# Kernel tuning notes

Hardware: AMD Instinct MI355X
Metric: run time of the kernel (lower is better)

## Reference

```python
import jax, jax.numpy as jnp
import numpy as np


def _gru(x, h, Wih, Whh, bih, bhh):
    # torch.nn.GRUCell math. x:(1,in), h:(1,H), Wih:(3H,in), Whh:(3H,H)
    gi = x @ Wih.T + bih
    gh = h @ Whh.T + bhh
    i_r, i_z, i_n = jnp.split(gi, 3, axis=-1)
    h_r, h_z, h_n = jnp.split(gh, 3, axis=-1)
    r = jax.nn.sigmoid(i_r + h_r)
    z = jax.nn.sigmoid(i_z + h_z)
    n = jnp.tanh(i_n + r * h_n)
    return (1.0 - z) * n + z * h


def _combine(S, Wa, ba, va):
    # SelfAttention.combine: additive attention over the stack axis.
    # S:(k,1,H), Wa:(H,A), ba:(A,), va:(A,)
    e = jnp.tanh(S @ Wa + ba) @ va          # (k,1) energies
    w = jax.nn.softmax(e, axis=0)            # softmax over stacked hidden states
    return jnp.sum(w[..., None] * S, axis=0)  # (1,H)


def setup_inputs() -> dict:
    key = jax.random.key(0)
    ks = jax.random.split(key, 20)
    T, F, H, A, L = 16384, 2048, 16, 64, 6
    G = 3 * H
    s = 0.1  # weight scale for numerical sanity
    return {
        "batch": jax.random.normal(ks[0], (T, 1, F), jnp.float32),
        "h0": jax.random.normal(ks[1], (L, 1, H), jnp.float32),
        "W_ih0": jax.random.normal(ks[2], (G, F), jnp.float32) * s,
        "W_hh0": jax.random.normal(ks[3], (G, H), jnp.float32) * s,
        "b_ih0": jax.random.normal(ks[4], (G,), jnp.float32) * s,
        "b_hh0": jax.random.normal(ks[5], (G,), jnp.float32) * s,
        "W_ih": jax.random.normal(ks[6], (L - 1, G, H), jnp.float32) * s,
        "W_hh": jax.random.normal(ks[7], (L - 1, G, H), jnp.float32) * s,
        "b_ih": jax.random.normal(ks[8], (L - 1, G), jnp.float32) * s,
        "b_hh": jax.random.normal(ks[9], (L - 1, G), jnp.float32) * s,
        "Wa": jax.random.normal(ks[10], (L, H, A), jnp.float32) * s,
        "ba": jax.random.normal(ks[11], (L, A), jnp.float32) * s,
        "va": jax.random.normal(ks[12], (L, A), jnp.float32) * s,
        "fc1_w": jax.random.normal(ks[13], (32, H), jnp.float32) * s,
        "fc1_b": jax.random.normal(ks[14], (32,), jnp.float32) * s,
        "fc2_w": jax.random.normal(ks[15], (1, 32), jnp.float32) * s,
        "fc2_b": jax.random.normal(ks[16], (1,), jnp.float32) * s,
    }


def reference(batch, h0, W_ih0, W_hh0, b_ih0, b_hh0, W_ih, W_hh, b_ih, b_hh,
              Wa, ba, va, fc1_w, fc1_b, fc2_w, fc2_b):
    L = Wa.shape[0]

    def step(h_s, x):
        # h_s: (L,1,H) carried hidden states, x: (1,F) current token
        inp = x.reshape(1, -1)
        new = []
        for l in range(L):
            if l == 0:
                inp = _gru(inp, h_s[0], W_ih0, W_hh0, b_ih0, b_hh0)
            else:
                inp = _gru(inp, h_s[l], W_ih[l - 1], W_hh[l - 1], b_ih[l - 1], b_hh[l - 1])
            new.append(inp)
        newS = jnp.stack(new)  # (L,1,H)
        # layer i attends over hidden states of layers i..L-1 (feedback combine)
        h_next = jnp.stack([_combine(newS[i:], Wa[i], ba[i], va[i]) for i in range(L)])
        top = h_next[-1].reshape(-1)  # (H,); dropout is identity in eval mode
        out = (top @ fc1_w.T + fc1_b) @ fc2_w.T + fc2_b  # (1,)
        return h_next, out

    _, outs = jax.lax.scan(step, h0, batch)
    return outs  # (T,1)
```

## Files before the change

kernel.cpp:

```cpp
#include <hip/hip_runtime.h>
#include <cstdint>
#include <cstddef>


#define TT 16384
#define FF 2048
#define HH 16
#define LL 6
#define GG 48
#define CHUNK 64
#define LOG2E 1.44269504088896340736f

__device__ float g_gi0p[(TT + CHUNK) * 64];

__device__ __forceinline__ float exp2_(float x) { return __builtin_amdgcn_exp2f(x); }
__device__ __forceinline__ float rcp_(float x) { return __builtin_amdgcn_rcpf(x); }
__device__ __forceinline__ float sig_n(float s) { return rcp_(1.f + exp2_(s)); }
__device__ __forceinline__ float tanh_p(float s) { return fmaf(-2.f, rcp_(exp2_(s) + 1.f), 1.f); }

#define MEMBAR() __asm__ __volatile__("" ::: "memory")

__device__ __forceinline__ float rdlane(float v, int l) {
  union { float f; int i; } a, b;
  a.f = v; b.i = __builtin_amdgcn_readlane(a.i, l); return b.f;
}
template <int CTRL>
__device__ __forceinline__ float dppf(float v) {
  union { float f; int i; } a, b;
  a.f = v; b.i = __builtin_amdgcn_mov_dpp(a.i, CTRL, 0xF, 0xF, true); return b.f;
}
template <int Q>
__device__ __forceinline__ float qbcast(float v) { return dppf<Q | (Q << 2) | (Q << 4) | (Q << 6)>(v); }

__device__ __forceinline__ float rowsum16(float v) {
  v += dppf<0xB1>(v);
  v += dppf<0x4E>(v);
  v += dppf<0x141>(v);
  v += dppf<0x140>(v);
  return v;
}
__device__ __forceinline__ float dot16r(const float (&w)[16], const float (&h)[16]) {
  float s0 = w[0] * h[0], s1 = w[1] * h[1], s2 = w[2] * h[2], s3 = w[3] * h[3];
#pragma unroll
  for (int k = 4; k < 16; k += 4) {
    s0 = fmaf(w[k], h[k], s0);       s1 = fmaf(w[k + 1], h[k + 1], s1);
    s2 = fmaf(w[k + 2], h[k + 2], s2); s3 = fmaf(w[k + 3], h[k + 3], s3);
  }
  return (s0 + s1) + (s2 + s3);
}
__device__ __forceinline__ float dot16i(const float (&w)[16], const float (&h)[16], float init) {
  float s0 = fmaf(w[0], h[0], init), s1 = w[1] * h[1], s2 = w[2] * h[2], s3 = w[3] * h[3];
#pragma unroll
  for (int k = 4; k < 16; k += 4) {
    s0 = fmaf(w[k], h[k], s0);       s1 = fmaf(w[k + 1], h[k + 1], s1);
    s2 = fmaf(w[k + 2], h[k + 2], s2); s3 = fmaf(w[k + 3], h[k + 3], s3);
  }
  return (s0 + s1) + (s2 + s3);
}

__device__ __forceinline__ void pollGE(int* f, int target) {
  while (__hip_atomic_load(f, __ATOMIC_ACQUIRE, __HIP_MEMORY_SCOPE_WORKGROUP) < target) {}
}
__device__ __forceinline__ void sigRel(int* f, int v) {
  __hip_atomic_store(f, v, __ATOMIC_RELAXED, __HIP_MEMORY_SCOPE_WORKGROUP);
}

__global__ __launch_bounds__(256) void gi0_gemm(const float* __restrict__ X,
                                                const float* __restrict__ W,
                                                const float* __restrict__ bias) {
  __shared__ float xs[64][132];
  __shared__ float ws[48][132];
  const int tid = threadIdx.x;
  const int t0 = blockIdx.x * 64;
  const int tg = tid & 15;
  const int tt = tid >> 4;
  float acc[4][3];
#pragma unroll
  for (int u = 0; u < 4; ++u)
#pragma unroll
    for (int v = 0; v < 3; ++v) acc[u][v] = 0.f;

  for (int k0 = 0; k0 < FF; k0 += 128) {
#pragma unroll
    for (int i = 0; i < 32; ++i) {
      int e = tid + 256 * i; int r = e >> 7, c = e & 127;
      xs[r][c] = X[(size_t)(t0 + r) * FF + k0 + c];
    }
#pragma unroll
    for (int i = 0; i < 24; ++i) {
      int e = tid + 256 * i; int r = e >> 7, c = e & 127;
      ws[r][c] = W[(size_t)r * FF + k0 + c];
    }
    __syncthreads();
#pragma unroll 8
    for (int c = 0; c < 128; ++c) {
      float x0 = xs[tt][c], x1 = xs[tt + 16][c], x2 = xs[tt + 32][c], x3 = xs[tt + 48][c];
      float w0 = ws[tg][c], w1 = ws[tg + 16][c], w2 = ws[tg + 32][c];
      acc[0][0] += x0 * w0; acc[0][1] += x0 * w1; acc[0][2] += x0 * w2;
      acc[1][0] += x1 * w0; acc[1][1] += x1 * w1; acc[1][2] += x1 * w2;
      acc[2][0] += x2 * w0; acc[2][1] += x2 * w1; acc[2][2] += x2 * w2;
      acc[3][0] += x3 * w0; acc[3][1] += x3 * w1; acc[3][2] += x3 * w2;
    }
    __syncthreads();
  }
  const float gsc3[3] = {-LOG2E, -LOG2E, 2.f * LOG2E};
#pragma unroll
  for (int u = 0; u < 4; ++u)
#pragma unroll
    for (int v = 0; v < 3; ++v)
      g_gi0p[(size_t)(t0 + tt + 16 * u) * 64 + tg * 4 + v] =
          (acc[u][v] + bias[tg + 16 * v]) * gsc3[v];
}

__global__ __launch_bounds__(512, 1) void fbrnn_scan(
    const float* __restrict__ h0,
    const float* __restrict__ Whh0, const float* __restrict__ bhh0,
    const float* __restrict__ Wih, const float* __restrict__ Whh,
    const float* __restrict__ bih, const float* __restrict__ bhh,
    const float* __restrict__ Wa, const float* __restrict__ ba,
    const float* __restrict__ va,
    const float* __restrict__ fc1w, const float* __restrict__ fc1b,
    const float* __restrict__ fc2w, const float* __restrict__ fc2b,
    float* __restrict__ out) {
  __shared__ __align__(16) float nsS[2][LL * HH];
  __shared__ __align__(16) float hS[2][5 * HH];
  __shared__ __align__(16) float ghS[2][5 * 64];
  __shared__ __align__(16) float nsOut[256 * HH];
  __shared__ __align__(16) float chunkS[2][CHUNK * 64];
  __shared__ int flagNs;
  __shared__ int cntC;
  __shared__ int flagChunk;
  __shared__ int flagOut;

  const int tid = threadIdx.x;
  const int wv = tid >> 6;
  const int lane = tid & 63;
  const int qg = lane & 3;
  const int kk = lane >> 2;
  const int k16 = lane & 15;
  const int gate = (qg < 3 ? qg : 2);
  const int G = gate * 16 + kk;
  const float gsc = (gate == 2) ? 2.f * LOG2E : -LOG2E;

  const bool isChain = (wv == 0);
  const bool isStream = (wv == 4);
  const bool isFc = (wv == 6);
  const bool isComb = !isChain && !isStream && !isFc;
  const int iw = (wv == 1) ? 0 : (wv == 2) ? 1 : (wv == 3) ? 2 : (wv == 7) ? 3 : 4;

  float WBih[5][16], bihR[5];
  float WB5[16];  float bhh5R = 0.f;
  float WaR[16], WhR[16];
  float baR = 0.f, vaR = 0.f, bhhR = 0.f;
  float fc1R[16];
  float fb1 = 0.f, fw2 = 0.f, fb2 = 0.f;

  if (isChain) {
#pragma unroll
    for (int l = 0; l < 5; ++l) {
#pragma unroll
      for (int k = 0; k < 16; ++k) WBih[l][k] = Wih[((l * GG) + G) * 16 + k] * gsc;
      bihR[l] = bih[l * GG + G] * gsc;
    }
#pragma unroll
    for (int k = 0; k < 16; ++k) WB5[k] = Whh[(4 * GG + G) * 16 + k] * gsc;
    bhh5R = bhh[4 * GG + G] * gsc;
  } else if (isComb) {
#pragma unroll
    for (int k = 0; k < 16; ++k) WaR[k] = Wa[(iw * 16 + k) * 64 + lane] * (2.f * LOG2E);
    baR = ba[iw * 64 + lane] * (2.f * LOG2E);
    vaR = va[iw * 64 + lane] * LOG2E;
    const float* wsrc = (iw == 0) ? (Whh0 + G * 16) : (Whh + ((iw - 1) * GG + G) * 16);
#pragma unroll
    for (int k = 0; k < 16; ++k) WhR[k] = wsrc[k] * gsc;
    bhhR = ((iw == 0) ? bhh0[G] : bhh[(iw - 1) * GG + G]) * gsc;
  } else if (isFc) {
    const int m = lane & 31;
#pragma unroll
    for (int k = 0; k < 16; ++k) fc1R[k] = fc1w[m * 16 + k];
    fb1 = fc1b[m]; fw2 = fc2w[m]; fb2 = fc2b[0];
  }

  if (tid == 0) { flagNs = 0; cntC = 0; flagChunk = 1; flagOut = 0; }

  float hv5 = 0.f, gh5reg = 0.f;
  if (isChain) {
    hv5 = h0[5 * 16 + kk];
    float hr[16];
#pragma unroll
    for (int k = 0; k < 16; ++k) hr[k] = h0[5 * 16 + k];
    gh5reg = dot16i(WB5, hr, bhh5R);
  } else if (isComb) {
    if (lane < 16) hS[1][iw * 16 + k16] = h0[iw * 16 + k16];
    float hr[16];
#pragma unroll
    for (int k = 0; k < 16; ++k) hr[k] = h0[iw * 16 + k];
    ghS[1][iw * 64 + lane] = dot16i(WhR, hr, bhhR);
  } else if (isStream) {
    const float4* src = (const float4*)g_gi0p;
    float4* dst = (float4*)(&chunkS[0][0]);
#pragma unroll
    for (int q = 0; q < 16; ++q) dst[q * 64 + lane] = src[q * 64 + lane];
  }
  __syncthreads();

  if (isStream) {
#pragma unroll 1
    for (int c = 1; c < 256; ++c) {
      if (c >= 2) pollGE(&flagNs, ((c - 1) * 64 - 1) * 8 + 1);
      const float4* src = (const float4*)(g_gi0p + ((size_t)c << 12));
      float4* dst = (float4*)(&chunkS[c & 1][0]);
#pragma unroll
      for (int q = 0; q < 16; ++q) dst[q * 64 + lane] = src[q * 64 + lane];
      MEMBAR();
      sigRel(&flagChunk, c + 1);
    }
    return;
  }

  if (isFc) {
    int fcc = 0;
#pragma unroll 1
    for (int t = 0; t < TT; ++t) {
      const int need = t * 8 + 6;
      if (fcc < need) {
        do {
          fcc = __hip_atomic_load(&flagNs, __ATOMIC_ACQUIRE, __HIP_MEMORY_SCOPE_WORKGROUP);
        } while (fcc < need);
      }
      const float4* np = (const float4*)(nsOut + (t & 255) * 16);
      float4 a0 = np[0], a1 = np[1], a2 = np[2], a3 = np[3];
      float nr[16] = {a0.x, a0.y, a0.z, a0.w, a1.x, a1.y, a1.z, a1.w,
                      a2.x, a2.y, a2.z, a2.w, a3.x, a3.y, a3.z, a3.w};
      float y = dot16i(fc1R, nr, fb1);
      float p = rowsum16(y * fw2);
      float o = rdlane(p, 0) + rdlane(p, 16) + fb2;
      if (lane == 0) out[t] = o;
      MEMBAR();
      sigRel(&flagOut, t + 1);
    }
    return;
  }

  if (isComb) {
    int fcache = 0;
#pragma unroll 1
    for (int t = 0; t < TT; ++t) {
      const int nb = t & 1;
      float S = 0.f, ha = 0.f, Pa = 0.f;
#pragma unroll
      for (int j = 0; j < 6; ++j) {
        if (j >= iw) {
          const int need = t * 8 + j + 1;
          if (fcache < need) {
            do {
              fcache = __hip_atomic_load(&flagNs, __ATOMIC_ACQUIRE, __HIP_MEMORY_SCOPE_WORKGROUP);
            } while (fcache < need);
          }
          const float4* np = (const float4*)(&nsS[nb][j * 16]);
          float4 a0 = np[0], a1 = np[1], a2 = np[2], a3 = np[3];
          float nr[16] = {a0.x, a0.y, a0.z, a0.w, a1.x, a1.y, a1.z, a1.w,
                          a2.x, a2.y, a2.z, a2.w, a3.x, a3.y, a3.z, a3.w};
          const float nsv = nsS[nb][j * 16 + k16];
          float u = dot16i(WaR, nr, baR);
          float pe = vaR * tanh_p(u);
          float P = dot16r(WhR, nr);
          float r = rowsum16(pe);
          float e = (rdlane(r, 0) + rdlane(r, 16)) + (rdlane(r, 32) + rdlane(r, 48));
          float w = exp2_(e);
          S += w; ha = fmaf(w, nsv, ha); Pa = fmaf(w, P, Pa);
        }
      }
      const float inv = rcp_(S);
      if (lane < 16) hS[nb][iw * 16 + k16] = ha * inv;
      ghS[nb][iw * 64 + lane] = fmaf(Pa, inv, bhhR);
      MEMBAR();
      if (lane == 0)
        __hip_atomic_fetch_add(&cntC, 1, __ATOMIC_RELAXED, __HIP_MEMORY_SCOPE_WORKGROUP);
    }
    return;
  }

  float gnext = chunkS[0][lane];
  float ns_sg[16];
  int ccache = 0;
#pragma unroll 1
  for (int t = 0; t < TT; ++t) {
    const int rb = (t + 1) & 1;
    const int wb = t & 1;

    const int cneed = 5 * t;
    if (ccache < cneed) {
      do {
        ccache = __hip_atomic_load(&cntC, __ATOMIC_ACQUIRE, __HIP_MEMORY_SCOPE_WORKGROUP);
      } while (ccache < cneed);
    }
    float ghv[6], hv[6];
#pragma unroll
    for (int l = 0; l < 5; ++l) { ghv[l] = ghS[rb][l * 64 + lane]; hv[l] = hS[rb][l * 16 + kk]; }
    ghv[5] = gh5reg; hv[5] = hv5;

    if ((t & 63) == 63) {
      const int cn = (t + 1) >> 6;
      if (cn < 256) pollGE(&flagChunk, cn + 1);
    }
    if ((t & 63) == 32) pollGE(&flagOut, t - 64);
    const float gpre = chunkS[((t + 1) >> 6) & 1][((t + 1) & 63) * 64 + lane];

    float ghb[6];
#pragma unroll
    for (int l = 1; l < 6; ++l) ghb[l] = ghv[l] + bihR[l - 1];

    float gi0v = gnext;
    float ns = 0.f;
#pragma unroll
    for (int l = 0; l < 6; ++l) {
      const float gh_g = ghv[l];
      const float s = (l == 0) ? (gi0v + gh_g) : dot16i(WBih[l - 1], ns_sg, ghb[l]);
      const float sg = sig_n(s);
      const float smg = s - gh_g;
      const float sr = qbcast<0>(sg);
      const float sz = qbcast<1>(sg);
      const float a = sz * hv[l];
      const float b = 1.f - sz;
      const float tq = tanh_p(fmaf(sr, gh_g, smg));
      ns = fmaf(tq, b, a);
      if (qg == 2) {
        nsS[wb][l * 16 + kk] = ns;
        if (l == 5) nsOut[(t & 255) * 16 + kk] = ns;
      }
      MEMBAR();
      if (l == 5 && lane == 0) sigRel(&flagNs, t * 8 + 6);
#pragma unroll
      for (int k = 0; k < 16; ++k) ns_sg[k] = rdlane(ns, 4 * k + 2);
      if (l < 5 && lane == 0) sigRel(&flagNs, t * 8 + l + 1);
    }
    hv5 = qbcast<2>(ns);
    gh5reg = dot16i(WB5, ns_sg, bhh5R);
    gnext = gpre;
  }
}

extern "C" void kernel_launch(void* const* d_in, const int* in_sizes, int n_in,
                              void* d_out, int out_size, void* d_ws, size_t ws_size,
                              hipStream_t stream) {
  const float* batch = (const float*)d_in[0];
  const float* h0    = (const float*)d_in[1];
  const float* Wih0  = (const float*)d_in[2];
  const float* Whh0  = (const float*)d_in[3];
  const float* bih0  = (const float*)d_in[4];
  const float* bhh0  = (const float*)d_in[5];
  const float* Wih   = (const float*)d_in[6];
  const float* Whh   = (const float*)d_in[7];
  const float* bih   = (const float*)d_in[8];
  const float* bhh   = (const float*)d_in[9];
  const float* Wa    = (const float*)d_in[10];
  const float* ba    = (const float*)d_in[11];
  const float* va    = (const float*)d_in[12];
  const float* fc1w  = (const float*)d_in[13];
  const float* fc1b  = (const float*)d_in[14];
  const float* fc2w  = (const float*)d_in[15];
  const float* fc2b  = (const float*)d_in[16];
  float* out = (float*)d_out;
  (void)in_sizes; (void)n_in; (void)out_size; (void)d_ws; (void)ws_size;

  gi0_gemm<<<TT / 64, 256, 0, stream>>>(batch, Wih0, bih0);
  fbrnn_scan<<<1, 512, 0, stream>>>(h0, Whh0, bhh0, Wih, Whh, bih, bhh,
                                    Wa, ba, va, fc1w, fc1b, fc2w, fc2b, out);
}
```

Baseline: 25.21 ms.

## Rebalance combine work across waves and replace counter sync with seqlock records

Combine waves for the lower layers now receive partial attention sums (over layers 0-2) that the fc and other waves compute early. The goal is to shorten the critical path after the last layer's state is produced. The shared counter plus separate hS/ghS buffers are replaced by float4 records with embedded generation tags, which the chain wave polls directly. A per-buffer gen5 flag signals the top-layer state. This removes the atomic fetch-add and the double-buffered read, but adds seqlock-style retry loops and more register pressure on the combine waves.

```diff
diff --git a/kernel.cpp b/kernel.cpp
--- a/kernel.cpp
+++ b/kernel.cpp
@@ -58,11 +58,33 @@
   return (s0 + s1) + (s2 + s3);
 }
 
+__device__ __forceinline__ int ldAcq(int* f) {
+  return __hip_atomic_load(f, __ATOMIC_ACQUIRE, __HIP_MEMORY_SCOPE_WORKGROUP);
+}
 __device__ __forceinline__ void pollGE(int* f, int target) {
-  while (__hip_atomic_load(f, __ATOMIC_ACQUIRE, __HIP_MEMORY_SCOPE_WORKGROUP) < target) {}
+  while (ldAcq(f) < target) {}
+}
+__device__ __forceinline__ void waitFlag(int* f, int& cache, int need) {
+  if (cache < need) { do { cache = ldAcq(f); } while (cache < need); }
 }
 __device__ __forceinline__ void sigRel(int* f, int v) {
   __hip_atomic_store(f, v, __ATOMIC_RELAXED, __HIP_MEMORY_SCOPE_WORKGROUP);
+}
+
+__device__ __forceinline__ void combBlock(const float4 A0, const float4 A1, const float4 A2,
+                                          const float4 A3, float nsv,
+                                          const float (&Wa)[16], float ba, float va,
+                                          const float (&Wh)[16],
+                                          float& S, float& ha, float& Pa) {
+  float nr[16] = {A0.x, A0.y, A0.z, A0.w, A1.x, A1.y, A1.z, A1.w,
+                  A2.x, A2.y, A2.z, A2.w, A3.x, A3.y, A3.z, A3.w};
+  float u = dot16i(Wa, nr, ba);
+  float P = dot16r(Wh, nr);
+  float pe = va * tanh_p(u);
+  float r = rowsum16(pe);
+  float e = (rdlane(r, 0) + rdlane(r, 16)) + (rdlane(r, 32) + rdlane(r, 48));
+  float w = exp2_(e);
+  S += w; ha = fmaf(w, nsv, ha); Pa = fmaf(w, P, Pa);
 }
 
 __global__ __launch_bounds__(256) void gi0_gemm(const float* __restrict__ X,
@@ -123,21 +145,20 @@
     const float* __restrict__ fc2w, const float* __restrict__ fc2b,
     float* __restrict__ out) {
   __shared__ __align__(16) float nsS[2][LL * HH];
-  __shared__ __align__(16) float hS[2][5 * HH];
-  __shared__ __align__(16) float ghS[2][5 * 64];
+  __shared__ __align__(16) float4 recS[5 * 64];
+  __shared__ __align__(16) float4 partS[3 * 64];
   __shared__ __align__(16) float nsOut[256 * HH];
   __shared__ __align__(16) float chunkS[2][CHUNK * 64];
   __shared__ int flagNs;
-  __shared__ int cntC;
   __shared__ int flagChunk;
   __shared__ int flagOut;
+  __shared__ int gen5[2];
 
   const int tid = threadIdx.x;
   const int wv = tid >> 6;
   const int lane = tid & 63;
   const int qg = lane & 3;
   const int kk = lane >> 2;
-  const int k16 = lane & 15;
   const int gate = (qg < 3 ? qg : 2);
   const int G = gate * 16 + kk;
   const float gsc = (gate == 2) ? 2.f * LOG2E : -LOG2E;
@@ -146,12 +167,15 @@
   const bool isStream = (wv == 4);
   const bool isFc = (wv == 6);
   const bool isComb = !isChain && !isStream && !isFc;
-  const int iw = (wv == 1) ? 0 : (wv == 2) ? 1 : (wv == 3) ? 2 : (wv == 7) ? 3 : 4;
+  const int pRow = (wv == 1) ? 0 : (wv == 2) ? 1 : (wv == 3) ? 2 : (wv == 7) ? 3 : 4;
+  const int hRow = (wv == 5) ? 1 : (wv == 7) ? 2 : (wv == 6) ? 0 : -1;
 
   float WBih[5][16], bihR[5];
   float WB5[16];  float bhh5R = 0.f;
-  float WaR[16], WhR[16];
-  float baR = 0.f, vaR = 0.f, bhhR = 0.f;
+  float WaP[16], WhP[16];
+  float baP = 0.f, vaP = 0.f, bhhP = 0.f;
+  float WaH[16], WhH[16];
+  float baH = 0.f, vaH = 0.f;
   float fc1R[16];
   float fb1 = 0.f, fw2 = 0.f, fb2 = 0.f;
 
@@ -165,23 +189,34 @@
 #pragma unroll
     for (int k = 0; k < 16; ++k) WB5[k] = Whh[(4 * GG + G) * 16 + k] * gsc;
     bhh5R = bhh[4 * GG + G] * gsc;
-  } else if (isComb) {
-#pragma unroll
-    for (int k = 0; k < 16; ++k) WaR[k] = Wa[(iw * 16 + k) * 64 + lane] * (2.f * LOG2E);
-    baR = ba[iw * 64 + lane] * (2.f * LOG2E);
-    vaR = va[iw * 64 + lane] * LOG2E;
-    const float* wsrc = (iw == 0) ? (Whh0 + G * 16) : (Whh + ((iw - 1) * GG + G) * 16);
-#pragma unroll
-    for (int k = 0; k < 16; ++k) WhR[k] = wsrc[k] * gsc;
-    bhhR = ((iw == 0) ? bhh0[G] : bhh[(iw - 1) * GG + G]) * gsc;
-  } else if (isFc) {
+  }
+  if (isComb) {
+#pragma unroll
+    for (int k = 0; k < 16; ++k) WaP[k] = Wa[(pRow * 16 + k) * 64 + lane] * (2.f * LOG2E);
+    baP = ba[pRow * 64 + lane] * (2.f * LOG2E);
+    vaP = va[pRow * 64 + lane] * LOG2E;
+    const float* ws = (pRow == 0) ? (Whh0 + G * 16) : (Whh + ((pRow - 1) * GG + G) * 16);
+#pragma unroll
+    for (int k = 0; k < 16; ++k) WhP[k] = ws[k] * gsc;
+    bhhP = ((pRow == 0) ? bhh0[G] : bhh[(pRow - 1) * GG + G]) * gsc;
+  }
+  if (hRow >= 0) {
+#pragma unroll
+    for (int k = 0; k < 16; ++k) WaH[k] = Wa[(hRow * 16 + k) * 64 + lane] * (2.f * LOG2E);
+    baH = ba[hRow * 64 + lane] * (2.f * LOG2E);
+    vaH = va[hRow * 64 + lane] * LOG2E;
+    const float* ws = (hRow == 0) ? (Whh0 + G * 16) : (Whh + ((hRow - 1) * GG + G) * 16);
+#pragma unroll
+    for (int k = 0; k < 16; ++k) WhH[k] = ws[k] * gsc;
+  }
+  if (isFc) {
     const int m = lane & 31;
 #pragma unroll
     for (int k = 0; k < 16; ++k) fc1R[k] = fc1w[m * 16 + k];
     fb1 = fc1b[m]; fw2 = fc2w[m]; fb2 = fc2b[0];
   }
 
-  if (tid == 0) { flagNs = 0; cntC = 0; flagChunk = 1; flagOut = 0; }
+  if (tid == 0) { flagNs = 0; flagChunk = 1; flagOut = 0; gen5[0] = 0; gen5[1] = 0; }
 
   float hv5 = 0.f, gh5reg = 0.f;
   if (isChain) {
@@ -191,18 +226,33 @@
     for (int k = 0; k < 16; ++k) hr[k] = h0[5 * 16 + k];
     gh5reg = dot16i(WB5, hr, bhh5R);
   } else if (isComb) {
-    if (lane < 16) hS[1][iw * 16 + k16] = h0[iw * 16 + k16];
     float hr[16];
 #pragma unroll
-    for (int k = 0; k < 16; ++k) hr[k] = h0[iw * 16 + k];
-    ghS[1][iw * 64 + lane] = dot16i(WhR, hr, bhhR);
+    for (int k = 0; k < 16; ++k) hr[k] = h0[pRow * 16 + k];
+    float4 rr;
+    rr.x = dot16i(WhP, hr, bhhP);
+    rr.y = h0[pRow * 16 + kk];
+    rr.z = __int_as_float(0);
+    rr.w = 0.f;
+    recS[pRow * 64 + lane] = rr;
   } else if (isStream) {
     const float4* src = (const float4*)g_gi0p;
     float4* dst = (float4*)(&chunkS[0][0]);
 #pragma unroll
     for (int q = 0; q < 16; ++q) dst[q * 64 + lane] = src[q * 64 + lane];
   }
+  if (wv == 6) partS[0 * 64 + lane] = make_float4(0.f, 0.f, 0.f, __int_as_float(0));
+  if (wv == 5) partS[1 * 64 + lane] = make_float4(0.f, 0.f, 0.f, __int_as_float(0));
+  if (wv == 7) partS[2 * 64 + lane] = make_float4(0.f, 0.f, 0.f, __int_as_float(0));
   __syncthreads();
+
+#define EBLOCK(J, WaX, baX, vaX, WhX, Sx, hax, Pax) do {                          \
+    waitFlag(&flagNs, fcache, t * 8 + (J) + 1);                                   \
+    const float4* np_ = (const float4*)&nsS[nb][(J) * 16];                        \
+    float4 A0_ = np_[0], A1_ = np_[1], A2_ = np_[2], A3_ = np_[3];                \
+    float nsv_ = nsS[nb][(J) * 16 + kk];                                          \
+    combBlock(A0_, A1_, A2_, A3_, nsv_, WaX, baX, vaX, WhX, Sx, hax, Pax);        \
+  } while (0)
 
   if (isStream) {
 #pragma unroll 1
@@ -219,15 +269,16 @@
   }
 
   if (isFc) {
-    int fcc = 0;
+    int fcache = 0;
 #pragma unroll 1
     for (int t = 0; t < TT; ++t) {
-      const int need = t * 8 + 6;
-      if (fcc < need) {
-        do {
-          fcc = __hip_atomic_load(&flagNs, __ATOMIC_ACQUIRE, __HIP_MEMORY_SCOPE_WORKGROUP);
-        } while (fcc < need);
-      }
+      const int nb = t & 1;
+      float Sh = 0.f, hah = 0.f, Pah = 0.f;
+      EBLOCK(0, WaH, baH, vaH, WhH, Sh, hah, Pah);
+      EBLOCK(1, WaH, baH, vaH, WhH, Sh, hah, Pah);
+      EBLOCK(2, WaH, baH, vaH, WhH, Sh, hah, Pah);
+      partS[0 * 64 + lane] = make_float4(Sh, hah, Pah, __int_as_float(t + 1));
+      waitFlag(&flagNs, fcache, t * 8 + 6);
       const float4* np = (const float4*)(nsOut + (t & 255) * 16);
       float4 a0 = np[0], a1 = np[1], a2 = np[2], a3 = np[3];
       float nr[16] = {a0.x, a0.y, a0.z, a0.w, a1.x, a1.y, a1.z, a1.w,
@@ -244,60 +295,112 @@
 
   if (isComb) {
     int fcache = 0;
-#pragma unroll 1
-    for (int t = 0; t < TT; ++t) {
-      const int nb = t & 1;
-      float S = 0.f, ha = 0.f, Pa = 0.f;
-#pragma unroll
-      for (int j = 0; j < 6; ++j) {
-        if (j >= iw) {
-          const int need = t * 8 + j + 1;
-          if (fcache < need) {
-            do {
-              fcache = __hip_atomic_load(&flagNs, __ATOMIC_ACQUIRE, __HIP_MEMORY_SCOPE_WORKGROUP);
-            } while (fcache < need);
-          }
-          const float4* np = (const float4*)(&nsS[nb][j * 16]);
-          float4 a0 = np[0], a1 = np[1], a2 = np[2], a3 = np[3];
-          float nr[16] = {a0.x, a0.y, a0.z, a0.w, a1.x, a1.y, a1.z, a1.w,
-                          a2.x, a2.y, a2.z, a2.w, a3.x, a3.y, a3.z, a3.w};
-          const float nsv = nsS[nb][j * 16 + k16];
-          float u = dot16i(WaR, nr, baR);
-          float pe = vaR * tanh_p(u);
-          float P = dot16r(WhR, nr);
-          float r = rowsum16(pe);
-          float e = (rdlane(r, 0) + rdlane(r, 16)) + (rdlane(r, 32) + rdlane(r, 48));
-          float w = exp2_(e);
-          S += w; ha = fmaf(w, nsv, ha); Pa = fmaf(w, P, Pa);
+    if (wv == 5) {
+#pragma unroll 1
+      for (int t = 0; t < TT; ++t) {
+        const int nb = t & 1;
+        const int tgt = t + 1;
+        float Sh = 0.f, hah = 0.f, Pah = 0.f;
+        EBLOCK(1, WaH, baH, vaH, WhH, Sh, hah, Pah);
+        EBLOCK(2, WaH, baH, vaH, WhH, Sh, hah, Pah);
+        partS[1 * 64 + lane] = make_float4(Sh, hah, Pah, __int_as_float(tgt));
+        float S = 0.f, ha = 0.f, Pa = 0.f;
+        EBLOCK(4, WaP, baP, vaP, WhP, S, ha, Pa);
+        float4 A0, A1, A2, A3; float nsv5;
+        for (;;) {
+          int g5 = ldAcq(&gen5[nb]);
+          MEMBAR();
+          const float4* np = (const float4*)&nsS[nb][5 * 16];
+          A0 = np[0]; A1 = np[1]; A2 = np[2]; A3 = np[3];
+          nsv5 = nsS[nb][5 * 16 + kk];
+          MEMBAR();
+          if (g5 >= tgt) break;
         }
+        combBlock(A0, A1, A2, A3, nsv5, WaP, baP, vaP, WhP, S, ha, Pa);
+        const float inv = rcp_(S);
+        float4 rr; rr.x = fmaf(Pa, inv, bhhP); rr.y = ha * inv;
+        rr.z = __int_as_float(tgt); rr.w = 0.f;
+        recS[4 * 64 + lane] = rr;
       }
-      const float inv = rcp_(S);
-      if (lane < 16) hS[nb][iw * 16 + k16] = ha * inv;
-      ghS[nb][iw * 64 + lane] = fmaf(Pa, inv, bhhR);
-      MEMBAR();
-      if (lane == 0)
-        __hip_atomic_fetch_add(&cntC, 1, __ATOMIC_RELAXED, __HIP_MEMORY_SCOPE_WORKGROUP);
+    } else if (wv == 7) {
+#pragma unroll 1
+      for (int t = 0; t < TT; ++t) {
+        const int nb = t & 1;
+        const int tgt = t + 1;
+        float Sh = 0.f, hah = 0.f, Pah = 0.f;
+        EBLOCK(2, WaH, baH, vaH, WhH, Sh, hah, Pah);
+        partS[2 * 64 + lane] = make_float4(Sh, hah, Pah, __int_as_float(tgt));
+        float S = 0.f, ha = 0.f, Pa = 0.f;
+        EBLOCK(3, WaP, baP, vaP, WhP, S, ha, Pa);
+        EBLOCK(4, WaP, baP, vaP, WhP, S, ha, Pa);
+        float4 A0, A1, A2, A3; float nsv5;
+        for (;;) {
+          int g5 = ldAcq(&gen5[nb]);
+          MEMBAR();
+          const float4* np = (const float4*)&nsS[nb][5 * 16];
+          A0 = np[0]; A1 = np[1]; A2 = np[2]; A3 = np[3];
+          nsv5 = nsS[nb][5 * 16 + kk];
+          MEMBAR();
+          if (g5 >= tgt) break;
+        }
+        combBlock(A0, A1, A2, A3, nsv5, WaP, baP, vaP, WhP, S, ha, Pa);
+        const float inv = rcp_(S);
+        float4 rr; rr.x = fmaf(Pa, inv, bhhP); rr.y = ha * inv;
+        rr.z = __int_as_float(tgt); rr.w = 0.f;
+        recS[3 * 64 + lane] = rr;
+      }
+    } else {
+#pragma unroll 1
+      for (int t = 0; t < TT; ++t) {
+        const int nb = t & 1;
+        const int tgt = t + 1;
+        float S = 0.f, ha = 0.f, Pa = 0.f;
+        EBLOCK(3, WaP, baP, vaP, WhP, S, ha, Pa);
+        EBLOCK(4, WaP, baP, vaP, WhP, S, ha, Pa);
+        float4 A0, A1, A2, A3, pp; float nsv5;
+        for (;;) {
+          int g5 = ldAcq(&gen5[nb]);
+          MEMBAR();
+          const float4* np = (const float4*)&nsS[nb][5 * 16];
+          A0 = np[0]; A1 = np[1]; A2 = np[2]; A3 = np[3];
+          nsv5 = nsS[nb][5 * 16 + kk];
+          pp = partS[pRow * 64 + lane];
+          MEMBAR();
+          int pok = __all(__float_as_int(pp.w) >= tgt);
+          if ((g5 >= tgt) & pok) break;
+        }
+        combBlock(A0, A1, A2, A3, nsv5, WaP, baP, vaP, WhP, S, ha, Pa);
+        S += pp.x; ha += pp.y; Pa += pp.z;
+        const float inv = rcp_(S);
+        float4 rr; rr.x = fmaf(Pa, inv, bhhP); rr.y = ha * inv;
+        rr.z = __int_as_float(tgt); rr.w = 0.f;
+        recS[pRow * 64 + lane] = rr;
+      }
     }
     return;
   }
 
   float gnext = chunkS[0][lane];
   float ns_sg[16];
-  int ccache = 0;
 #pragma unroll 1
   for (int t = 0; t < TT; ++t) {
-    const int rb = (t + 1) & 1;
     const int wb = t & 1;
 
-    const int cneed = 5 * t;
-    if (ccache < cneed) {
-      do {
-        ccache = __hip_atomic_load(&cntC, __ATOMIC_ACQUIRE, __HIP_MEMORY_SCOPE_WORKGROUP);
-      } while (ccache < cneed);
+    float4 r0, r1, r2, r3, r4;
+    for (;;) {
+      MEMBAR();
+      r0 = recS[0 * 64 + lane]; r1 = recS[1 * 64 + lane]; r2 = recS[2 * 64 + lane];
+      r3 = recS[3 * 64 + lane]; r4 = recS[4 * 64 + lane];
+      MEMBAR();
+      int c = (__float_as_int(r0.z) >= t) & (__float_as_int(r1.z) >= t) &
+              (__float_as_int(r2.z) >= t) & (__float_as_int(r3.z) >= t) &
+              (__float_as_int(r4.z) >= t);
+      if (__all(c)) break;
     }
     float ghv[6], hv[6];
-#pragma unroll
-    for (int l = 0; l < 5; ++l) { ghv[l] = ghS[rb][l * 64 + lane]; hv[l] = hS[rb][l * 16 + kk]; }
+    ghv[0] = r0.x; hv[0] = r0.y; ghv[1] = r1.x; hv[1] = r1.y;
+    ghv[2] = r2.x; hv[2] = r2.y; ghv[3] = r3.x; hv[3] = r3.y;
+    ghv[4] = r4.x; hv[4] = r4.y;
     ghv[5] = gh5reg; hv[5] = hv5;
 
     if ((t & 63) == 63) {
@@ -330,7 +433,7 @@
         if (l == 5) nsOut[(t & 255) * 16 + kk] = ns;
       }
       MEMBAR();
-      if (l == 5 && lane == 0) sigRel(&flagNs, t * 8 + 6);
+      if (l == 5 && lane == 0) { sigRel(&gen5[wb], t + 1); sigRel(&flagNs, t * 8 + 6); }
 #pragma unroll
       for (int k = 0; k < 16; ++k) ns_sg[k] = rdlane(ns, 4 * k + 2);
       if (l < 5 && lane == 0) sigRel(&flagNs, t * 8 + l + 1);
```

Result: no change. 24.99 ms (-0.9%).
